# Kernel tuning notes

Measured on AMD Instinct MI355X. Metric: run time of the kernel, lower is better.

## Reference

```python
import jax, jax.numpy as jnp
import numpy as np

B, S, D, NH = 2, 1024, 2048, 8
QK, V, I = 1024, 2048, 8192  # qk_dim = D/2, v_dim = D, intermediate = 4D
CAP = 15.0
EPS = 1e-6


def setup_inputs() -> dict:
    key = jax.random.key(0)
    ks = jax.random.split(key, 12)
    sc = D ** -0.5
    return {
        "x": jax.random.normal(ks[0], (B, S, D), jnp.float32),
        "Wq": jax.random.normal(ks[1], (D, QK), jnp.float32) * sc,
        "Wk": jax.random.normal(ks[2], (D, QK), jnp.float32) * sc,
        "Wv": jax.random.normal(ks[3], (D, V), jnp.float32) * sc,
        "Wo": jax.random.normal(ks[4], (D, V), jnp.float32) * sc,
        "Wi": jax.random.normal(ks[5], (D, NH), jnp.float32) * sc,
        "bi": -10.0 * jnp.ones((NH,), jnp.float32),   # xLSTM input-gate bias init
        "Wf": jax.random.normal(ks[6], (D, NH), jnp.float32) * sc,
        "bf": jnp.linspace(3.0, 6.0, NH, dtype=jnp.float32),  # forget-gate bias init
        "mh_norm_w": jnp.ones((V,), jnp.float32),
        "Wout": jax.random.normal(ks[7], (V, D), jnp.float32) * (V ** -0.5),
        "rms1_w": jnp.ones((D,), jnp.float32),
        "Wgate": jax.random.normal(ks[8], (D, I), jnp.float32) * sc,
        "Wup": jax.random.normal(ks[9], (D, I), jnp.float32) * sc,
        "Wdown": jax.random.normal(ks[10], (I, D), jnp.float32) * (I ** -0.5),
        "rms2_w": jnp.ones((D,), jnp.float32),
    }


def soft_cap(x, cap=CAP):
    return cap * jnp.tanh(x / cap)


def rms_norm(x, w, eps=EPS):
    xf = x.astype(jnp.float32)
    var = jnp.mean(xf * xf, axis=-1, keepdims=True)
    return (w * (xf * jax.lax.rsqrt(var + eps))).astype(x.dtype)


def mlstm_stabilized(q, k, v, i, f):
    # q,k: [B,NH,S,DQK]; v: [B,NH,S,DV]; i,f: [B,NH,S] (soft-capped preacts)
    dqk = q.shape[-1]
    logf = jax.nn.log_sigmoid(f.astype(jnp.float32))
    lfc = jnp.cumsum(logf, axis=-1)                         # [B,NH,S]
    tri = jnp.tril(jnp.ones((S, S), bool))
    # log decay D[t,s] = sum_{j=s+1..t} log sig(f_j) + i_s  (causal)
    logD = jnp.where(tri, lfc[..., :, None] - lfc[..., None, :], -jnp.inf) + i[..., None, :]
    m = jnp.max(logD, axis=-1, keepdims=True)               # [B,NH,S,1] stabilizer
    Dm = jnp.exp(logD - m)
    scores = jnp.einsum("bhsd,bhtd->bhst", q, k) * (dqk ** -0.5) * Dm
    n = jnp.maximum(jnp.abs(scores.sum(-1, keepdims=True)), jnp.exp(-m))
    return jnp.einsum("bhst,bhtv->bhsv", scores, v) / (n + EPS)  # [B,NH,S,DV]


def xlstm_layer(x, Wq, Wk, Wv, Wo, Wi, bi, Wf, bf, mh_norm_w, Wout):
    q = (x @ Wq).reshape(B, S, NH, -1).transpose(0, 2, 1, 3)
    k = (x @ Wk).reshape(B, S, NH, -1).transpose(0, 2, 1, 3)
    v = (x @ Wv).reshape(B, S, NH, -1).transpose(0, 2, 1, 3)
    o_preact = x @ Wo                                       # [B,S,V]
    i = soft_cap(x @ Wi + bi).transpose(0, 2, 1)            # [B,NH,S]
    f = soft_cap(x @ Wf + bf).transpose(0, 2, 1)
    h = mlstm_stabilized(q, k, v, i, f)                     # [B,NH,S,DV]
    h = h.transpose(0, 2, 1, 3)                             # [B,S,NH,DV]
    # multi-head RMS norm over per-head value dim
    hf = h.astype(jnp.float32)
    var = jnp.mean(hf * hf, axis=-1, keepdims=True)
    hn = (hf * jax.lax.rsqrt(var + EPS)).reshape(B, S, V) * mh_norm_w
    h_out = jax.nn.sigmoid(o_preact) * hn                   # output gate
    return h_out @ Wout


def reference(x, Wq, Wk, Wv, Wo, Wi, bi, Wf, bf, mh_norm_w, Wout, rms1_w,
              Wgate, Wup, Wdown, rms2_w):
    residual = x
    h = xlstm_layer(x, Wq, Wk, Wv, Wo, Wi, bi, Wf, bf, mh_norm_w, Wout)
    h = residual + rms_norm(h, rms1_w)
    mlp = (jax.nn.silu(h @ Wgate) * (h @ Wup)) @ Wdown
    return h + rms_norm(mlp, rms2_w)
```

## Files before the change

### kernel.cpp

```cpp
#include <hip/hip_runtime.h>
#include <hip/hip_bf16.h>

#define TOKENS 2048
#define DMODEL 2048
#define SEQ    1024

typedef __attribute__((ext_vector_type(8))) short bf16x8;
typedef __attribute__((ext_vector_type(4))) short bf16x4;
typedef __attribute__((ext_vector_type(4))) float f32x4;
typedef __attribute__((ext_vector_type(8))) unsigned short u16x8;
typedef __attribute__((ext_vector_type(4))) unsigned short u16x4;

__device__ __forceinline__ float sigmoidf_(float x) { return 1.f / (1.f + expf(-x)); }
__device__ __forceinline__ float softcapf_(float x) { return 15.f * tanhf(x * (1.f / 15.f)); }
__device__ __forceinline__ float logsigf_(float x) {
  return (x >= 0.f) ? -log1pf(expf(-x)) : (x - log1pf(expf(x)));
}
__device__ __forceinline__ unsigned short f2bf(float f) {
  unsigned u = __builtin_bit_cast(unsigned, f);
  u += 0x7FFFu + ((u >> 16) & 1u);
  return (unsigned short)(u >> 16);
}
__device__ __forceinline__ float bf2f(unsigned short b) {
  unsigned u = ((unsigned)b) << 16;
  return __builtin_bit_cast(float, u);
}

typedef __attribute__((address_space(3))) void lds_void;
typedef const __attribute__((address_space(1))) void gmem_void;
__device__ __forceinline__ void gload16(const void* g, void* l) {
  __builtin_amdgcn_global_load_lds((gmem_void*)g, (lds_void*)l, 16, 0, 0);
}
__device__ __forceinline__ unsigned lds_off(const void* p) {
  return (unsigned)(size_t)(__attribute__((address_space(3))) const void*)p;
}

#if defined(__has_builtin)
#if __has_builtin(__builtin_amdgcn_mfma_f32_16x16x16bf16_1k)
#define HAVE_MFMA16 1
#endif
#endif

__device__ __forceinline__ f32x4 mfma16_bf16(bf16x4 a, bf16x4 b, f32x4 c) {
#ifdef HAVE_MFMA16
  return __builtin_amdgcn_mfma_f32_16x16x16bf16_1k(a, b, c, 0, 0, 0);
#else
  f32x4 d;
  asm volatile("v_mfma_f32_16x16x16_bf16 %0, %1, %2, %3"
               : "=v"(d) : "v"(a), "v"(b), "v"(c));
  return d;
#endif
}

__device__ __forceinline__ bf16x4 tr_read(unsigned addr) {
  bf16x4 d;
  asm volatile("ds_read_b64_tr_b16 %0, %1" : "=v"(d) : "v"(addr));
  return d;
}

__device__ __forceinline__ void remap_block(int& bm, int& bn) {
  const int nbx = gridDim.x, nby = gridDim.y;
  const int bid = blockIdx.y * nbx + blockIdx.x;
  const int q = (nbx * nby) >> 3;
  const int lid = (bid & 7) * q + (bid >> 3);
  bm = lid % nby;
  bn = lid / nby;
}

template <int EPI>
__global__ __launch_bounds__(512, 2) void gemm256(
    const unsigned short* __restrict__ A, const unsigned short* __restrict__ BT,
    void* __restrict__ Cout, void* __restrict__ Cout2,
    const unsigned short* __restrict__ aux, int M, int N, int K, int ldk) {
  __shared__ unsigned short lds[2][2][8192];
  const int tid = threadIdx.x;
  int bm, bn;
  remap_block(bm, bn);
  const int m0 = bm * 256, n0 = bn * 256;
  const int wid = tid >> 6, lane = tid & 63;
  const int wr = wid >> 2, wc = wid & 3;
  const int fr = lane & 15, fq = lane >> 4;
  const size_t kz = (size_t)blockIdx.z * K;

  const f32x4 zero = {0.f, 0.f, 0.f, 0.f};
  f32x4 acc[8][4];
#pragma unroll
  for (int m = 0; m < 8; ++m)
#pragma unroll
    for (int n = 0; n < 4; ++n) acc[m][n] = zero;

  const int sr = tid >> 2;
  const int sc = tid & 3;
  const int sgc = sc ^ ((sr + (sr >> 2)) & 3);
  const unsigned short* Asrc = A + kz + (size_t)(m0 + sr) * ldk + sgc * 8;
  const unsigned short* Bsrc = BT + kz + (size_t)(n0 + sr) * ldk + sgc * 8;
  const size_t hstep = (size_t)128 * ldk;
  const int ldst = sr * 32 + sc * 8;

  const int rsw = (fq ^ ((fr + (fr >> 2)) & 3)) * 8;
  const int arow0 = wr * 128 + fr;
  const int brow0 = wc * 64 + fr;

  auto stage = [&](int t) {
    const size_t ko = (size_t)t * 32;
    const int bs = t & 1;
    gload16(Asrc + ko, &lds[bs][0][ldst]);
    gload16(Asrc + ko + hstep, &lds[bs][0][4096 + ldst]);
    gload16(Bsrc + ko, &lds[bs][1][ldst]);
    gload16(Bsrc + ko + hstep, &lds[bs][1][4096 + ldst]);
  };

  const int NT = K >> 5;
  stage(0);
  asm volatile("s_waitcnt vmcnt(0)" ::: "memory");
  __builtin_amdgcn_s_barrier();

  for (int t = 0; t < NT; ++t) {
    const int b = t & 1;
    if (t + 1 < NT) stage(t + 1);
    const unsigned short* la = &lds[b][0][0];
    const unsigned short* lb = &lds[b][1][0];
    bf16x8 bfm[4], af[4];
#pragma unroll
    for (int n = 0; n < 4; ++n)
      bfm[n] = *(const bf16x8*)&lb[(brow0 + n * 16) * 32 + rsw];
#pragma unroll
    for (int m = 0; m < 4; ++m)
      af[m] = *(const bf16x8*)&la[(arow0 + m * 16) * 32 + rsw];
    __builtin_amdgcn_s_setprio(1);
#pragma unroll
    for (int m = 0; m < 4; ++m)
#pragma unroll
      for (int n = 0; n < 4; ++n)
        acc[m][n] = __builtin_amdgcn_mfma_f32_16x16x32_bf16(af[m], bfm[n],
                                                            acc[m][n], 0, 0, 0);
    __builtin_amdgcn_s_setprio(0);
#pragma unroll
    for (int m = 0; m < 4; ++m)
      af[m] = *(const bf16x8*)&la[(arow0 + 64 + m * 16) * 32 + rsw];
    __builtin_amdgcn_s_setprio(1);
#pragma unroll
    for (int m = 0; m < 4; ++m)
#pragma unroll
      for (int n = 0; n < 4; ++n)
        acc[4 + m][n] = __builtin_amdgcn_mfma_f32_16x16x32_bf16(
            af[m], bfm[n], acc[4 + m][n], 0, 0, 0);
    __builtin_amdgcn_s_setprio(0);
    asm volatile("s_waitcnt vmcnt(0)" ::: "memory");
    __builtin_amdgcn_s_barrier();
  }

  const int orow = m0 + wr * 128 + fq * 4;
  const int ocol = n0 + wc * 64 + fr;
#pragma unroll
  for (int m = 0; m < 8; ++m) {
#pragma unroll
    for (int n = 0; n < 4; ++n) {
      const int cc = ocol + n * 16;
#pragma unroll
      for (int j = 0; j < 4; ++j) {
        const int r = orow + m * 16 + j;
        float v = acc[m][n][j];
        if (EPI == 0) {
          ((float*)Cout + (size_t)blockIdx.z * M * N)[(size_t)r * N + cc] = v;
        } else if (EPI == 1) {
          ((unsigned short*)Cout)[(size_t)r * N + cc] = f2bf(v);
        } else if (EPI == 2) {
          const size_t idx = (size_t)r * N + cc;
          const float gv = bf2f(aux[idx]);
          ((unsigned short*)Cout)[idx] = f2bf(v * gv * sigmoidf_(gv));
        } else {
          if (cc < 2048)
            ((unsigned short*)Cout)[(size_t)r * 2048 + cc] = f2bf(v);
          else
            ((float*)Cout2)[(size_t)r * 2048 + cc - 2048] = v;
        }
      }
    }
  }
}

template <int EPI>
__global__ __launch_bounds__(256) void gemm_bf16(
    const unsigned short* __restrict__ A, const unsigned short* __restrict__ BT,
    void* __restrict__ Cout, int M, int N, int K) {
  __shared__ unsigned short As[2][128 * 32];
  __shared__ unsigned short Bs[2][128 * 32];
  const int tid = threadIdx.x;
  int bm, bn;
  remap_block(bm, bn);
  const int m0 = bm * 128;
  const int n0 = bn * 128;
  const int wid = tid >> 6;
  const int lane = tid & 63;
  const int wr = wid >> 1, wc = wid & 1;
  const int fr = lane & 15, fq = lane >> 4;

  const f32x4 zero = {0.f, 0.f, 0.f, 0.f};
  f32x4 acc[4][4];
#pragma unroll
  for (int m = 0; m < 4; ++m)
#pragma unroll
    for (int n = 0; n < 4; ++n) acc[m][n] = zero;

  const int srow = tid >> 2;
  const int sc = tid & 3;
  const int sgc = sc ^ ((srow + (srow >> 2)) & 3);
  const int scol = sgc * 8;
  const unsigned short* Ag0 = A + (size_t)(m0 + srow) * K + scol;
  const unsigned short* Ag1 = A + (size_t)(m0 + 64 + srow) * K + scol;
  const unsigned short* Bg0 = BT + (size_t)(n0 + srow) * K + scol;
  const unsigned short* Bg1 = BT + (size_t)(n0 + 64 + srow) * K + scol;
  const int rsw = (fq ^ ((fr + (fr >> 2)) & 3)) * 8;

  gload16(Ag0, &As[0][tid * 8]);
  gload16(Ag1, &As[0][2048 + tid * 8]);
  gload16(Bg0, &Bs[0][tid * 8]);
  gload16(Bg1, &Bs[0][2048 + tid * 8]);
  __syncthreads();

  const int nt = K >> 5;
  for (int t = 0; t < nt; ++t) {
    const int cur = t & 1;
    if (t + 1 < nt) {
      const int k0 = (t + 1) << 5;
      gload16(Ag0 + k0, &As[cur ^ 1][tid * 8]);
      gload16(Ag1 + k0, &As[cur ^ 1][2048 + tid * 8]);
      gload16(Bg0 + k0, &Bs[cur ^ 1][tid * 8]);
      gload16(Bg1 + k0, &Bs[cur ^ 1][2048 + tid * 8]);
    }
    bf16x8 af[4], bfm[4];
#pragma unroll
    for (int m = 0; m < 4; ++m)
      af[m] = *(const bf16x8*)&As[cur][(wr * 64 + m * 16 + fr) * 32 + rsw];
#pragma unroll
    for (int n = 0; n < 4; ++n)
      bfm[n] = *(const bf16x8*)&Bs[cur][(wc * 64 + n * 16 + fr) * 32 + rsw];
    __builtin_amdgcn_s_setprio(1);
#pragma unroll
    for (int m = 0; m < 4; ++m)
#pragma unroll
      for (int n = 0; n < 4; ++n)
        acc[m][n] = __builtin_amdgcn_mfma_f32_16x16x32_bf16(af[m], bfm[n],
                                                            acc[m][n], 0, 0, 0);
    __builtin_amdgcn_s_setprio(0);
    __syncthreads();
  }

  const int orow = m0 + wr * 64 + fq * 4;
  const int ocol = n0 + wc * 64 + fr;
#pragma unroll
  for (int m = 0; m < 4; ++m) {
#pragma unroll
    for (int n = 0; n < 4; ++n) {
      const int cc = ocol + n * 16;
#pragma unroll
      for (int j = 0; j < 4; ++j) {
        const int r = orow + m * 16 + j;
        float v = acc[m][n][j];
        if (EPI == 0) ((float*)Cout)[(size_t)r * N + cc] = v;
        else ((unsigned short*)Cout)[(size_t)r * N + cc] = f2bf(v);
      }
    }
  }
}

__global__ __launch_bounds__(256) void castf2b_kernel(
    const float* __restrict__ in, unsigned short* __restrict__ outp) {
  const size_t i = ((size_t)blockIdx.x * 256 + threadIdx.x) * 8;
  float4 a = *(const float4*)&in[i];
  float4 b = *(const float4*)&in[i + 4];
  u16x8 o;
  o[0] = f2bf(a.x); o[1] = f2bf(a.y); o[2] = f2bf(a.z); o[3] = f2bf(a.w);
  o[4] = f2bf(b.x); o[5] = f2bf(b.y); o[6] = f2bf(b.z); o[7] = f2bf(b.w);
  *(u16x8*)&outp[i] = o;
}

__global__ __launch_bounds__(256) void castT_kernel(
    const float* __restrict__ W, unsigned short* __restrict__ WT, int K, int N) {
  __shared__ float tile[32][33];
  const int n0 = blockIdx.x * 32, k0 = blockIdx.y * 32;
  const int r = threadIdx.x >> 3;
  const int c4 = (threadIdx.x & 7) * 4;
  float4 v = *(const float4*)&W[(size_t)(k0 + r) * N + n0 + c4];
  tile[r][c4 + 0] = v.x; tile[r][c4 + 1] = v.y;
  tile[r][c4 + 2] = v.z; tile[r][c4 + 3] = v.w;
  __syncthreads();
  u16x4 o;
  o[0] = f2bf(tile[c4 + 0][r]); o[1] = f2bf(tile[c4 + 1][r]);
  o[2] = f2bf(tile[c4 + 2][r]); o[3] = f2bf(tile[c4 + 3][r]);
  *(u16x4*)&WT[(size_t)(n0 + r) * K + k0 + c4] = o;
}

__global__ __launch_bounds__(256) void gatesT_kernel(
    const float* __restrict__ Wi, const float* __restrict__ Wf,
    float* __restrict__ WT) {
  const int idx = blockIdx.x * 256 + threadIdx.x;
  const int row = idx >> 11;
  const int d = idx & 2047;
  const float* W = (row < 8) ? Wi : Wf;
  WT[idx] = W[d * 8 + (row & 7)];
}

__global__ __launch_bounds__(256) void gates_kernel(
    const float* __restrict__ x, const float* __restrict__ WT,
    const float* __restrict__ bi, const float* __restrict__ bf,
    float* __restrict__ icap, float* __restrict__ fls) {
  const int t = blockIdx.x;
  const int tid = threadIdx.x;
  __shared__ float xs[2048];
  *(float4*)&xs[tid * 4] = *(const float4*)&x[(size_t)t * 2048 + tid * 4];
  *(float4*)&xs[1024 + tid * 4] =
      *(const float4*)&x[(size_t)t * 2048 + 1024 + tid * 4];
  __syncthreads();
  const int wave = tid >> 6, lane = tid & 63;
  const int b = t >> 10, s = t & 1023;
  for (int gg = wave; gg < 16; gg += 4) {
    const int head = gg & 7;
    const int isF = gg >> 3;
    const float* Wrow = WT + (size_t)gg * 2048;
    float acc = 0.f;
#pragma unroll
    for (int it = 0; it < 8; ++it) {
      const float4 w4 = *(const float4*)&Wrow[it * 256 + lane * 4];
      const float4 x4 = *(const float4*)&xs[it * 256 + lane * 4];
      acc = fmaf(x4.x, w4.x, acc);
      acc = fmaf(x4.y, w4.y, acc);
      acc = fmaf(x4.z, w4.z, acc);
      acc = fmaf(x4.w, w4.w, acc);
    }
#pragma unroll
    for (int m = 32; m > 0; m >>= 1) acc += __shfl_down(acc, m, 64);
    if (lane == 0) {
      const size_t o = (size_t)(b * 8 + head) * 1024 + s;
      if (isF) fls[o] = logsigf_(softcapf_(acc + bf[head]));
      else icap[o] = softcapf_(acc + bi[head]);
    }
  }
}

__global__ __launch_bounds__(1024) void scan_kernel(
    const float* __restrict__ icap, const float* __restrict__ fls,
    float* __restrict__ lfc, float* __restrict__ garr, float* __restrict__ mx) {
  const int bh = blockIdx.x;
  const int tid = threadIdx.x;
  __shared__ float sm[1024];
  sm[tid] = fls[(size_t)bh * 1024 + tid];
  __syncthreads();
  for (int off = 1; off < 1024; off <<= 1) {
    float v = sm[tid];
    if (tid >= off) v += sm[tid - off];
    __syncthreads();
    sm[tid] = v;
    __syncthreads();
  }
  const float l = sm[tid];
  lfc[(size_t)bh * 1024 + tid] = l;
  const float g = icap[(size_t)bh * 1024 + tid] - l;
  garr[(size_t)bh * 1024 + tid] = g;
  __syncthreads();
  sm[tid] = g;
  __syncthreads();
  for (int off = 1; off < 1024; off <<= 1) {
    float v = sm[tid];
    if (tid >= off) v = fmaxf(v, sm[tid - off]);
    __syncthreads();
    sm[tid] = v;
    __syncthreads();
  }
  mx[(size_t)bh * 1024 + tid] = sm[tid];
}

__global__ __launch_bounds__(128) void mlstm_mfma_kernel(
    const unsigned short* __restrict__ qkb, const unsigned short* __restrict__ vb,
    const float* __restrict__ garr, const float* __restrict__ lfc,
    const float* __restrict__ mx, float* __restrict__ h) {
  __shared__ unsigned short k_lds[32 * 128];
  __shared__ unsigned short v_lds[32 * 256];
  const int tid = threadIdx.x;
  const int lane = tid & 63;
  const int w = tid >> 6;
  const int bh = blockIdx.y;
  const int b = bh >> 3, hh = bh & 7;
  const int tb = blockIdx.x;
  const int fr = lane & 15, fq = lane >> 4;
  const int tw = tb * 32 + w * 16 + fr;
  const size_t tokT = (size_t)(b * SEQ + tw);
  const float scale = 0.08838834764831845f;

  bf16x8 qf[4];
#pragma unroll
  for (int kd = 0; kd < 4; ++kd)
    qf[kd] = *(const bf16x8*)&qkb[tokT * 2048 + hh * 128 + kd * 32 + fq * 8];

  const float Mt = mx[(size_t)bh * SEQ + tw];
  const float mt = lfc[(size_t)bh * SEQ + tw] + Mt;

  f32x4 acc[16];
  const f32x4 zero = {0.f, 0.f, 0.f, 0.f};
#pragma unroll
  for (int D = 0; D < 16; ++D) acc[D] = zero;
  float asum = 0.f;

  const unsigned vbase = lds_off(v_lds);
  const int nsb = tb + 1;

  for (int sb = 0; sb < nsb; ++sb) {
    const int s0 = sb * 32;
    if (sb) __syncthreads();
#pragma unroll
    for (int it = 0; it < 4; ++it) {
      const int ck = it * 128 + tid;
      const int s = ck >> 4, c = ck & 15;
      const int cg = c ^ (s & 7);
      gload16(&qkb[(size_t)(b * SEQ + s0 + s) * 2048 + 1024 + hh * 128 + cg * 8],
              &k_lds[ck * 8]);
    }
#pragma unroll
    for (int it = 0; it < 8; ++it) {
      const int cv = it * 128 + tid;
      const int W_ = cv >> 9, D = (cv >> 5) & 15, g = (cv >> 3) & 3,
                jj = (cv >> 1) & 3, c2 = cv & 1;
      const int s = W_ * 16 + g * 4 + jj;
      gload16(&vb[(size_t)(b * SEQ + s0 + s) * 2048 + hh * 256 + D * 16 + c2 * 8],
              &v_lds[cv * 8]);
    }
    __syncthreads();

#pragma unroll
    for (int st = 0; st < 2; ++st) {
      f32x4 cfrag = zero;
      const int srow = st * 16 + fr;
#pragma unroll
      for (int kd = 0; kd < 4; ++kd) {
        const int cc = (kd * 4 + fq) ^ (srow & 7);
        const bf16x8 kf = *(const bf16x8*)&k_lds[srow * 128 + cc * 8];
        cfrag = __builtin_amdgcn_mfma_f32_16x16x32_bf16(kf, qf[kd], cfrag, 0, 0, 0);
      }
      const int sbase = s0 + st * 16 + fq * 4;
      const float4 g4 = *(const float4*)&garr[(size_t)bh * SEQ + sbase];
      float wv[4];
      wv[0] = (sbase + 0 <= tw) ? cfrag[0] * scale * __expf(g4.x - Mt) : 0.f;
      wv[1] = (sbase + 1 <= tw) ? cfrag[1] * scale * __expf(g4.y - Mt) : 0.f;
      wv[2] = (sbase + 2 <= tw) ? cfrag[2] * scale * __expf(g4.z - Mt) : 0.f;
      wv[3] = (sbase + 3 <= tw) ? cfrag[3] * scale * __expf(g4.w - Mt) : 0.f;
      asum += wv[0] + wv[1] + wv[2] + wv[3];
      bf16x4 pf;
      pf[0] = (short)f2bf(wv[0]); pf[1] = (short)f2bf(wv[1]);
      pf[2] = (short)f2bf(wv[2]); pf[3] = (short)f2bf(wv[3]);

#pragma unroll
      for (int Dg = 0; Dg < 2; ++Dg) {
        bf16x4 vf[8];
#pragma unroll
        for (int D = 0; D < 8; ++D)
          vf[D] = tr_read(vbase + (st * 4096 + (Dg * 8 + D) * 256) * 2 + lane * 8);
        asm volatile("s_waitcnt lgkmcnt(0)" ::: "memory");
        __builtin_amdgcn_sched_barrier(0);
#pragma unroll
        for (int D = 0; D < 8; ++D)
          acc[Dg * 8 + D] = mfma16_bf16(vf[D], pf, acc[Dg * 8 + D]);
      }
    }
  }

  asum += __shfl_xor(asum, 16, 64);
  asum += __shfl_xor(asum, 32, 64);
  const float n = fmaxf(fabsf(asum), __expf(-mt));
  const float inv = 1.f / (n + 1e-6f);
  asm volatile("s_nop 7\n\ts_nop 7" ::);
  float* hrow = &h[tokT * 2048 + hh * 256];
#pragma unroll
  for (int D = 0; D < 16; ++D) {
    float4 o4;
    o4.x = acc[D][0] * inv;
    o4.y = acc[D][1] * inv;
    o4.z = acc[D][2] * inv;
    o4.w = acc[D][3] * inv;
    *(float4*)&hrow[D * 16 + fq * 4] = o4;
  }
}

__global__ __launch_bounds__(256) void hout_kernel(
    const float* __restrict__ h, const float* __restrict__ obuf,
    const float* __restrict__ mhw, unsigned short* __restrict__ houtb) {
  const int t = blockIdx.x;
  const int tid = threadIdx.x;
  const size_t base = (size_t)t * 2048 + tid * 8;
  float vals[8];
  *(float4*)&vals[0] = *(const float4*)&h[base];
  *(float4*)&vals[4] = *(const float4*)&h[base + 4];
  float ss = 0.f;
#pragma unroll
  for (int j = 0; j < 8; ++j) ss += vals[j] * vals[j];
#pragma unroll
  for (int m = 16; m > 0; m >>= 1) ss += __shfl_xor(ss, m, 32);
  const float rinv = rsqrtf(ss * (1.f / 256.f) + 1e-6f);
  float ov[8];
  *(float4*)&ov[0] = *(const float4*)&obuf[base];
  *(float4*)&ov[4] = *(const float4*)&obuf[base + 4];
  u16x8 res;
#pragma unroll
  for (int j = 0; j < 8; ++j) {
    const float hn = vals[j] * rinv * mhw[tid * 8 + j];
    res[j] = f2bf(hn * sigmoidf_(ov[j]));
  }
  *(u16x8*)&houtb[base] = res;
}

template <int EMIT_BF16, int NY>
__global__ __launch_bounds__(256) void addrms_kernel(
    const float* __restrict__ base_, const float* __restrict__ y0,
    const float* __restrict__ y1, const float* __restrict__ y2,
    const float* __restrict__ y3, const float* __restrict__ w,
    float* __restrict__ outp, unsigned short* __restrict__ outb) {
  const int t = blockIdx.x;
  const int tid = threadIdx.x;
  __shared__ float red[4];
  const size_t boff = (size_t)t * 2048 + tid * 8;
  float vals[8];
  *(float4*)&vals[0] = *(const float4*)&y0[boff];
  *(float4*)&vals[4] = *(const float4*)&y0[boff + 4];
  if (NY == 4) {
    float v1[8];
    *(float4*)&v1[0] = *(const float4*)&y1[boff];
    *(float4*)&v1[4] = *(const float4*)&y1[boff + 4];
#pragma unroll
    for (int j = 0; j < 8; ++j) vals[j] += v1[j];
    *(float4*)&v1[0] = *(const float4*)&y2[boff];
    *(float4*)&v1[4] = *(const float4*)&y2[boff + 4];
#pragma unroll
    for (int j = 0; j < 8; ++j) vals[j] += v1[j];
    *(float4*)&v1[0] = *(const float4*)&y3[boff];
    *(float4*)&v1[4] = *(const float4*)&y3[boff + 4];
#pragma unroll
    for (int j = 0; j < 8; ++j) vals[j] += v1[j];
  }
  float ss = 0.f;
#pragma unroll
  for (int j = 0; j < 8; ++j) ss += vals[j] * vals[j];
#pragma unroll
  for (int m = 32; m > 0; m >>= 1) ss += __shfl_xor(ss, m, 64);
  if ((tid & 63) == 0) red[tid >> 6] = ss;
  __syncthreads();
  ss = red[0] + red[1] + red[2] + red[3];
  const float rinv = rsqrtf(ss * (1.f / 2048.f) + 1e-6f);
  float bv[8];
  *(float4*)&bv[0] = *(const float4*)&base_[boff];
  *(float4*)&bv[4] = *(const float4*)&base_[boff + 4];
  float res[8];
  u16x8 rb;
#pragma unroll
  for (int j = 0; j < 8; ++j) {
    res[j] = bv[j] + vals[j] * rinv * w[tid * 8 + j];
    if (EMIT_BF16) rb[j] = f2bf(res[j]);
  }
  *(float4*)&outp[boff] = *(float4*)&res[0];
  *(float4*)&outp[boff + 4] = *(float4*)&res[4];
  if (EMIT_BF16) *(u16x8*)&outb[boff] = rb;
}

extern "C" void kernel_launch(void* const* d_in, const int* in_sizes, int n_in,
                              void* d_out, int out_size, void* d_ws,
                              size_t ws_size, hipStream_t stream) {
  const float* x = (const float*)d_in[0];
  const float* Wq = (const float*)d_in[1];
  const float* Wk = (const float*)d_in[2];
  const float* Wv = (const float*)d_in[3];
  const float* Wo = (const float*)d_in[4];
  const float* Wi = (const float*)d_in[5];
  const float* bi = (const float*)d_in[6];
  const float* Wf = (const float*)d_in[7];
  const float* bf = (const float*)d_in[8];
  const float* mhw = (const float*)d_in[9];
  const float* Wout = (const float*)d_in[10];
  const float* rms1 = (const float*)d_in[11];
  const float* Wgate = (const float*)d_in[12];
  const float* Wup = (const float*)d_in[13];
  const float* Wdown = (const float*)d_in[14];
  const float* rms2 = (const float*)d_in[15];
  float* out = (float*)d_out;
  char* base = (char*)d_ws;
  const size_t MBy = 1024 * 1024;

  unsigned short* W = (unsigned short*)(base);
  float* obuf = (float*)(base + 32 * MBy);
  unsigned short* actb = (unsigned short*)(base + 32 * MBy);
  float* gs = (float*)(base + 48 * MBy);
  unsigned short* houtb = (unsigned short*)(base + 48 * MBy);
  float* h = (float*)(base + 64 * MBy);
  float* f1 = (float*)(base + 64 * MBy);
  unsigned short* gbuf = (unsigned short*)(base + 80 * MBy);
  float* mlp = (float*)(base + 80 * MBy);
  unsigned short* xb = (unsigned short*)(base + 112 * MBy);
  unsigned short* f1b = (unsigned short*)(base + 112 * MBy);
  unsigned short* qkb = (unsigned short*)(base + 120 * MBy);
  float* attn = (float*)(base + 120 * MBy);
  unsigned short* vb = (unsigned short*)(base + 128 * MBy);
  float* icap = gs;
  float* fls = gs + 16384;
  float* lfc = gs + 32768;
  float* garr = gs + 49152;
  float* mxp = gs + 65536;
  float* gwT = gs + 81920;

  const dim3 blk(256);

  castf2b_kernel<<<TOKENS, blk, 0, stream>>>(x, xb);
  gatesT_kernel<<<128, blk, 0, stream>>>(Wi, Wf, gwT);
  gates_kernel<<<TOKENS, blk, 0, stream>>>(x, gwT, bi, bf, icap, fls);
  scan_kernel<<<16, 1024, 0, stream>>>(icap, fls, lfc, garr, mxp);

  castT_kernel<<<dim3(32, 64), blk, 0, stream>>>(Wq, W, 2048, 1024);
  castT_kernel<<<dim3(32, 64), blk, 0, stream>>>(Wk, W + 1024 * 2048, 2048, 1024);
  gemm_bf16<1><<<dim3(16, 16), blk, 0, stream>>>(xb, W, qkb, TOKENS, 2048, 2048);

  castT_kernel<<<dim3(64, 64), blk, 0, stream>>>(Wv, W, 2048, 2048);
  castT_kernel<<<dim3(64, 64), blk, 0, stream>>>(Wo, W + 2048 * 2048, 2048, 2048);
  gemm256<3><<<dim3(16, 8), dim3(512), 0, stream>>>(
      xb, W, vb, obuf, nullptr, TOKENS, 4096, 2048, 2048);

  mlstm_mfma_kernel<<<dim3(32, 16), dim3(128), 0, stream>>>(qkb, vb, garr, lfc,
                                                            mxp, h);
  hout_kernel<<<TOKENS, blk, 0, stream>>>(h, obuf, mhw, houtb);

  castT_kernel<<<dim3(64, 64), blk, 0, stream>>>(Wout, W, 2048, 2048);
  gemm_bf16<0><<<dim3(16, 16), blk, 0, stream>>>(houtb, W, attn, TOKENS, 2048,
                                                 2048);

  addrms_kernel<1, 1><<<TOKENS, blk, 0, stream>>>(
      x, attn, nullptr, nullptr, nullptr, rms1, f1, f1b);

  castT_kernel<<<dim3(256, 64), blk, 0, stream>>>(Wgate, W, 2048, 8192);
  gemm256<1><<<dim3(32, 8), dim3(512), 0, stream>>>(
      f1b, W, gbuf, nullptr, nullptr, TOKENS, 8192, 2048, 2048);
  castT_kernel<<<dim3(256, 64), blk, 0, stream>>>(Wup, W, 2048, 8192);
  gemm256<2><<<dim3(32, 8), dim3(512), 0, stream>>>(
      f1b, W, actb, nullptr, gbuf, TOKENS, 8192, 2048, 2048);

  castT_kernel<<<dim3(64, 256), blk, 0, stream>>>(Wdown, W, 8192, 2048);
  gemm256<0><<<dim3(8, 8, 4), dim3(512), 0, stream>>>(
      actb, W, mlp, nullptr, nullptr, TOKENS, 2048, 2048, 8192);

  addrms_kernel<0, 4><<<TOKENS, blk, 0, stream>>>(
      f1, mlp, mlp + 4194304, mlp + 8388608, mlp + 12582912, rms2, out,
      nullptr);
}
```

Before: 582.6 us.

## Triple-buffer gemm256 pipeline, fuse QKVO projections, widen weight transpose-cast tiles

The 256-tile GEMM moves from double to triple LDS buffering with two stages in flight and a single barrier per iteration, so global loads are hidden better behind the MFMA work. The Q/K and V/O projections are merged into one 6144-wide GEMM whose epilogue splits its output into qk, v and o buffers, replacing the separate 128-tile GEMM for QK. The transpose-cast kernel now processes 64x32 tiles and writes 16-byte vectors. The extra LDS buffer and the dropped occupancy hint in launch bounds may reduce occupancy.

```diff
diff --git a/kernel.cpp b/kernel.cpp
--- a/kernel.cpp
+++ b/kernel.cpp
@@ -68,11 +68,11 @@
 }
 
 template <int EPI>
-__global__ __launch_bounds__(512, 2) void gemm256(
+__global__ __launch_bounds__(512) void gemm256(
     const unsigned short* __restrict__ A, const unsigned short* __restrict__ BT,
-    void* __restrict__ Cout, void* __restrict__ Cout2,
+    void* __restrict__ Cout, void* __restrict__ Cout2, void* __restrict__ Cout3,
     const unsigned short* __restrict__ aux, int M, int N, int K, int ldk) {
-  __shared__ unsigned short lds[2][2][8192];
+  __shared__ unsigned short lds[3][2][8192];
   const int tid = threadIdx.x;
   int bm, bn;
   remap_block(bm, bn);
@@ -103,7 +103,7 @@
 
   auto stage = [&](int t) {
     const size_t ko = (size_t)t * 32;
-    const int bs = t & 1;
+    const int bs = t % 3;
     gload16(Asrc + ko, &lds[bs][0][ldst]);
     gload16(Asrc + ko + hstep, &lds[bs][0][4096 + ldst]);
     gload16(Bsrc + ko, &lds[bs][1][ldst]);
@@ -112,12 +112,17 @@
 
   const int NT = K >> 5;
   stage(0);
-  asm volatile("s_waitcnt vmcnt(0)" ::: "memory");
-  __builtin_amdgcn_s_barrier();
+  stage(1);
 
   for (int t = 0; t < NT; ++t) {
-    const int b = t & 1;
-    if (t + 1 < NT) stage(t + 1);
+    if (t + 1 < NT) {
+      asm volatile("s_waitcnt vmcnt(4)" ::: "memory");
+    } else {
+      asm volatile("s_waitcnt vmcnt(0)" ::: "memory");
+    }
+    __builtin_amdgcn_s_barrier();
+    if (t + 2 < NT) stage(t + 2);
+    const int b = t % 3;
     const unsigned short* la = &lds[b][0][0];
     const unsigned short* lb = &lds[b][1][0];
     bf16x8 bfm[4], af[4];
@@ -146,8 +151,6 @@
         acc[4 + m][n] = __builtin_amdgcn_mfma_f32_16x16x32_bf16(
             af[m], bfm[n], acc[4 + m][n], 0, 0, 0);
     __builtin_amdgcn_s_setprio(0);
-    asm volatile("s_waitcnt vmcnt(0)" ::: "memory");
-    __builtin_amdgcn_s_barrier();
   }
 
   const int orow = m0 + wr * 128 + fq * 4;
@@ -172,8 +175,10 @@
         } else {
           if (cc < 2048)
             ((unsigned short*)Cout)[(size_t)r * 2048 + cc] = f2bf(v);
+          else if (cc < 4096)
+            ((unsigned short*)Cout2)[(size_t)r * 2048 + cc - 2048] = f2bf(v);
           else
-            ((float*)Cout2)[(size_t)r * 2048 + cc - 2048] = v;
+            ((float*)Cout3)[(size_t)r * 2048 + cc - 4096] = v;
         }
       }
     }
@@ -278,18 +283,23 @@
 
 __global__ __launch_bounds__(256) void castT_kernel(
     const float* __restrict__ W, unsigned short* __restrict__ WT, int K, int N) {
-  __shared__ float tile[32][33];
-  const int n0 = blockIdx.x * 32, k0 = blockIdx.y * 32;
+  __shared__ float tile[64][33];
+  const int n0 = blockIdx.x * 32, k0 = blockIdx.y * 64;
   const int r = threadIdx.x >> 3;
   const int c4 = (threadIdx.x & 7) * 4;
-  float4 v = *(const float4*)&W[(size_t)(k0 + r) * N + n0 + c4];
-  tile[r][c4 + 0] = v.x; tile[r][c4 + 1] = v.y;
-  tile[r][c4 + 2] = v.z; tile[r][c4 + 3] = v.w;
+  float4 v0 = *(const float4*)&W[(size_t)(k0 + r) * N + n0 + c4];
+  float4 v1 = *(const float4*)&W[(size_t)(k0 + 32 + r) * N + n0 + c4];
+  tile[r][c4 + 0] = v0.x; tile[r][c4 + 1] = v0.y;
+  tile[r][c4 + 2] = v0.z; tile[r][c4 + 3] = v0.w;
+  tile[r + 32][c4 + 0] = v1.x; tile[r + 32][c4 + 1] = v1.y;
+  tile[r + 32][c4 + 2] = v1.z; tile[r + 32][c4 + 3] = v1.w;
   __syncthreads();
-  u16x4 o;
-  o[0] = f2bf(tile[c4 + 0][r]); o[1] = f2bf(tile[c4 + 1][r]);
-  o[2] = f2bf(tile[c4 + 2][r]); o[3] = f2bf(tile[c4 + 3][r]);
-  *(u16x4*)&WT[(size_t)(n0 + r) * K + k0 + c4] = o;
+  const int n = threadIdx.x >> 3;
+  const int kc = (threadIdx.x & 7) * 8;
+  u16x8 o;
+#pragma unroll
+  for (int j = 0; j < 8; ++j) o[j] = f2bf(tile[kc + j][n]);
+  *(u16x8*)&WT[(size_t)(n0 + n) * K + k0 + kc] = o;
 }
 
 __global__ __launch_bounds__(256) void gatesT_kernel(
@@ -611,36 +621,37 @@
   gates_kernel<<<TOKENS, blk, 0, stream>>>(x, gwT, bi, bf, icap, fls);
   scan_kernel<<<16, 1024, 0, stream>>>(icap, fls, lfc, garr, mxp);
 
-  castT_kernel<<<dim3(32, 64), blk, 0, stream>>>(Wq, W, 2048, 1024);
-  castT_kernel<<<dim3(32, 64), blk, 0, stream>>>(Wk, W + 1024 * 2048, 2048, 1024);
-  gemm_bf16<1><<<dim3(16, 16), blk, 0, stream>>>(xb, W, qkb, TOKENS, 2048, 2048);
-
-  castT_kernel<<<dim3(64, 64), blk, 0, stream>>>(Wv, W, 2048, 2048);
-  castT_kernel<<<dim3(64, 64), blk, 0, stream>>>(Wo, W + 2048 * 2048, 2048, 2048);
-  gemm256<3><<<dim3(16, 8), dim3(512), 0, stream>>>(
-      xb, W, vb, obuf, nullptr, TOKENS, 4096, 2048, 2048);
+  castT_kernel<<<dim3(32, 32), blk, 0, stream>>>(Wq, W, 2048, 1024);
+  castT_kernel<<<dim3(32, 32), blk, 0, stream>>>(Wk, W + (size_t)1024 * 2048,
+                                                 2048, 1024);
+  castT_kernel<<<dim3(64, 32), blk, 0, stream>>>(Wv, W + (size_t)2048 * 2048,
+                                                 2048, 2048);
+  castT_kernel<<<dim3(64, 32), blk, 0, stream>>>(Wo, W + (size_t)4096 * 2048,
+                                                 2048, 2048);
+  gemm256<4><<<dim3(24, 8), dim3(512), 0, stream>>>(
+      xb, W, qkb, vb, obuf, nullptr, TOKENS, 6144, 2048, 2048);
 
   mlstm_mfma_kernel<<<dim3(32, 16), dim3(128), 0, stream>>>(qkb, vb, garr, lfc,
                                                             mxp, h);
   hout_kernel<<<TOKENS, blk, 0, stream>>>(h, obuf, mhw, houtb);
 
-  castT_kernel<<<dim3(64, 64), blk, 0, stream>>>(Wout, W, 2048, 2048);
+  castT_kernel<<<dim3(64, 32), blk, 0, stream>>>(Wout, W, 2048, 2048);
   gemm_bf16<0><<<dim3(16, 16), blk, 0, stream>>>(houtb, W, attn, TOKENS, 2048,
                                                  2048);
 
   addrms_kernel<1, 1><<<TOKENS, blk, 0, stream>>>(
       x, attn, nullptr, nullptr, nullptr, rms1, f1, f1b);
 
-  castT_kernel<<<dim3(256, 64), blk, 0, stream>>>(Wgate, W, 2048, 8192);
+  castT_kernel<<<dim3(256, 32), blk, 0, stream>>>(Wgate, W, 2048, 8192);
   gemm256<1><<<dim3(32, 8), dim3(512), 0, stream>>>(
-      f1b, W, gbuf, nullptr, nullptr, TOKENS, 8192, 2048, 2048);
-  castT_kernel<<<dim3(256, 64), blk, 0, stream>>>(Wup, W, 2048, 8192);
+      f1b, W, gbuf, nullptr, nullptr, nullptr, TOKENS, 8192, 2048, 2048);
+  castT_kernel<<<dim3(256, 32), blk, 0, stream>>>(Wup, W, 2048, 8192);
   gemm256<2><<<dim3(32, 8), dim3(512), 0, stream>>>(
-      f1b, W, actb, nullptr, gbuf, TOKENS, 8192, 2048, 2048);
-
-  castT_kernel<<<dim3(64, 256), blk, 0, stream>>>(Wdown, W, 8192, 2048);
+      f1b, W, actb, nullptr, nullptr, gbuf, TOKENS, 8192, 2048, 2048);
+
+  castT_kernel<<<dim3(64, 128), blk, 0, stream>>>(Wdown, W, 8192, 2048);
   gemm256<0><<<dim3(8, 8, 4), dim3(512), 0, stream>>>(
-      actb, W, mlp, nullptr, nullptr, TOKENS, 2048, 2048, 8192);
+      actb, W, mlp, nullptr, nullptr, nullptr, TOKENS, 2048, 2048, 8192);
 
   addrms_kernel<0, 4><<<TOKENS, blk, 0, stream>>>(
       f1, mlp, mlp + 4194304, mlp + 8388608, mlp + 12582912, rms2, out,
```

New measurement: 534.0 us. 8.3% less time.
